# Kernel optimization log

Hardware: AMD Instinct MI355X
Metric: run time of the kernel (lower is better)

Reference implementation:

```python
import jax, jax.numpy as jnp
import numpy as np

V, T_CTX, D, H, L = 32000, 1024, 768, 12, 6
K = D // H  # head_size = 64
EPS = 1e-5


def _ln(x, g, b):
    mu = jnp.mean(x, axis=-1, keepdims=True)
    var = jnp.mean((x - mu) ** 2, axis=-1, keepdims=True)
    return (x - mu) / jnp.sqrt(var + EPS) * g + b


def setup_inputs() -> dict:
    key = jax.random.key(0)
    ks = jax.random.split(key, 24)
    std = 0.02
    B, T = 4, 1024
    inp = {
        "token_ids": jax.random.randint(ks[0], (B, T), 0, V),
        "targets": jax.random.randint(ks[1], (B, T), 0, V),
        "tok_emb": std * jax.random.normal(ks[2], (V, D), jnp.float32),
        "pos_emb": std * jax.random.normal(ks[3], (T_CTX, D), jnp.float32),
        # per-layer stacked params
        "Wq": std * jax.random.normal(ks[4], (L, H, D, K), jnp.float32),
        "Wk": std * jax.random.normal(ks[5], (L, H, D, K), jnp.float32),
        "Wv": std * jax.random.normal(ks[6], (L, H, D, D), jnp.float32),
        "Wproj": std * jax.random.normal(ks[7], (L, H * D, D), jnp.float32),
        "bproj": jnp.zeros((L, D), jnp.float32),
        "ln1_g": jnp.ones((L, D), jnp.float32),
        "ln1_b": jnp.zeros((L, D), jnp.float32),
        "ln2_g": jnp.ones((L, D), jnp.float32),
        "ln2_b": jnp.zeros((L, D), jnp.float32),
        "W1": std * jax.random.normal(ks[8], (L, D, 4 * D), jnp.float32),
        "b1": jnp.zeros((L, 4 * D), jnp.float32),
        "W2": std * jax.random.normal(ks[9], (L, 4 * D, D), jnp.float32),
        "b2": jnp.zeros((L, D), jnp.float32),
        "lnf_g": jnp.ones((D,), jnp.float32),
        "lnf_b": jnp.zeros((D,), jnp.float32),
        "Whead": std * jax.random.normal(ks[10], (D, V), jnp.float32),
        "bhead": jnp.zeros((V,), jnp.float32),
    }
    return inp


def reference(token_ids, targets, tok_emb, pos_emb, Wq, Wk, Wv, Wproj, bproj,
              ln1_g, ln1_b, ln2_g, ln2_b, W1, b1, W2, b2, lnf_g, lnf_b,
              Whead, bhead):
    B, T = token_ids.shape
    x = tok_emb[token_ids] + pos_emb[:T]  # (B,T,D)
    mask = jnp.tril(jnp.ones((T, T), bool))  # causal tril buffer
    scale = 1.0 / np.sqrt(K)
    for l in range(L):
        h = _ln(x, ln1_g[l], ln1_b[l])
        q = jnp.einsum("btd,hdk->bhtk", h, Wq[l])
        k = jnp.einsum("btd,hdk->bhtk", h, Wk[l])
        v = jnp.einsum("btd,hde->bhte", h, Wv[l])  # value proj is D->D per head
        s = jnp.einsum("bhtk,bhsk->bhts", q, k) * scale
        s = jnp.where(mask, s, -jnp.inf)
        a = jax.nn.softmax(s, axis=-1)
        o = jnp.einsum("bhts,bhse->bhte", a, v)  # (B,H,T,D)
        o = o.transpose(0, 2, 1, 3).reshape(B, T, H * D)  # concat heads
        x = x + o @ Wproj[l] + bproj[l]
        h2 = _ln(x, ln2_g[l], ln2_b[l])
        x = x + jax.nn.relu(h2 @ W1[l] + b1[l]) @ W2[l] + b2[l]
    x = _ln(x, lnf_g, lnf_b)
    logits = x @ Whead + bhead  # (B,T,V)
    logp = jax.nn.log_softmax(logits, axis=-1)
    loss = -jnp.take_along_axis(logp, targets[..., None], axis=-1).mean()
    return logits, loss
```

## Files before the change

### kernel.cpp

```cpp
#include <hip/hip_runtime.h>
#include <hip/hip_bf16.h>


#define NBATCH 4
#define TT 1024
#define DD 768
#define NH 12
#define HK 64
#define NL 6
#define NV 32000
#define BT 4096
#define HD 9216
#define FF 3072

using bf16x8 = __attribute__((ext_vector_type(8))) short;
using f32x4  = __attribute__((ext_vector_type(4))) float;

#define GF_OUTBF16 1
#define GF_ACCUM   2
#define GF_BIAS    4
#define GF_RELU    8

__global__ __launch_bounds__(256, 2)
void gemm_kernel(const __hip_bfloat16* __restrict__ A,
                 const __hip_bfloat16* __restrict__ Bt,
                 void* __restrict__ Cv,
                 const float* __restrict__ bias,
                 int Kd, int lda, int ldb, int ldc,
                 int GH,
                 long sA1, long sA2, long sB1, long sB2, long sC1, long sC2,
                 int flags, float scale)
{
    int g  = blockIdx.z;
    int g1 = g / GH, g2 = g % GH;
    const short* Ag = (const short*)A  + g1 * sA1 + g2 * sA2;
    const short* Bg = (const short*)Bt + g1 * sB1 + g2 * sB2;
    long coff = g1 * sC1 + g2 * sC2;
    int n0 = blockIdx.x * 128, m0 = blockIdx.y * 128;

    __shared__ short As[128 * 40];
    __shared__ short Bs[128 * 40];

    int tid  = threadIdx.x;
    int wave = tid >> 6, lane = tid & 63;
    int wm = (wave >> 1) * 64, wn = (wave & 1) * 64;
    int lm = lane & 15, quad = lane >> 4;

    f32x4 acc[4][4];
#pragma unroll
    for (int i = 0; i < 4; i++)
#pragma unroll
        for (int j = 0; j < 4; j++) acc[i][j] = (f32x4){0.f, 0.f, 0.f, 0.f};

    for (int k0 = 0; k0 < Kd; k0 += 32) {
        __syncthreads();
#pragma unroll
        for (int i = 0; i < 2; i++) {
            int c = tid + i * 256;
            int row = c >> 2, kc = (c & 3) << 3;
            *(bf16x8*)(&As[row * 40 + kc]) =
                *(const bf16x8*)(Ag + (long)(m0 + row) * lda + k0 + kc);
            *(bf16x8*)(&Bs[row * 40 + kc]) =
                *(const bf16x8*)(Bg + (long)(n0 + row) * ldb + k0 + kc);
        }
        __syncthreads();

        bf16x8 af[4], bfv[4];
#pragma unroll
        for (int mi = 0; mi < 4; mi++)
            af[mi] = *(const bf16x8*)(&As[(wm + mi * 16 + lm) * 40 + quad * 8]);
#pragma unroll
        for (int ni = 0; ni < 4; ni++)
            bfv[ni] = *(const bf16x8*)(&Bs[(wn + ni * 16 + lm) * 40 + quad * 8]);
#pragma unroll
        for (int mi = 0; mi < 4; mi++)
#pragma unroll
            for (int ni = 0; ni < 4; ni++)
                acc[mi][ni] = __builtin_amdgcn_mfma_f32_16x16x32_bf16(
                    af[mi], bfv[ni], acc[mi][ni], 0, 0, 0);
    }

    bool outbf = flags & GF_OUTBF16;
    bool accum = flags & GF_ACCUM;
    bool hbias = flags & GF_BIAS;
    bool relu  = flags & GF_RELU;
#pragma unroll
    for (int mi = 0; mi < 4; mi++) {
#pragma unroll
        for (int ni = 0; ni < 4; ni++) {
            int colg = n0 + wn + ni * 16 + lm;
            float bv = hbias ? bias[colg] : 0.f;
#pragma unroll
            for (int r = 0; r < 4; r++) {
                int rowg = m0 + wm + mi * 16 + quad * 4 + r;
                float v = acc[mi][ni][r] * scale + bv;
                if (relu) v = fmaxf(v, 0.f);
                long idx = coff + (long)rowg * ldc + colg;
                if (outbf) {
                    ((__hip_bfloat16*)Cv)[idx] = __float2bfloat16(v);
                } else {
                    float* cp = (float*)Cv + idx;
                    *cp = accum ? (*cp + v) : v;
                }
            }
        }
    }
}

__global__ void transpose_kernel(const float* __restrict__ in,
                                 __hip_bfloat16* __restrict__ out,
                                 int R, int C, long inBatch, long outBatch)
{
    __shared__ float tile[32][33];
    long ib = (long)blockIdx.z * inBatch;
    long ob = (long)blockIdx.z * outBatch;
    int c0 = blockIdx.x * 32, r0 = blockIdx.y * 32;
    int tx = threadIdx.x, ty = threadIdx.y;
#pragma unroll
    for (int i = 0; i < 4; i++) {
        int r = r0 + ty + i * 8;
        tile[ty + i * 8][tx] = in[ib + (long)r * C + c0 + tx];
    }
    __syncthreads();
#pragma unroll
    for (int i = 0; i < 4; i++) {
        int c = c0 + ty + i * 8;
        out[ob + (long)c * R + r0 + tx] = __float2bfloat16(tile[tx][ty + i * 8]);
    }
}

__global__ void ln_kernel(const float* __restrict__ x,
                          const float* __restrict__ g,
                          const float* __restrict__ b,
                          __hip_bfloat16* __restrict__ out)
{
    int row = blockIdx.x;
    const float* xp = x + (long)row * DD;
    int tid = threadIdx.x;
    float a0 = xp[tid], a1 = xp[tid + 256], a2 = xp[tid + 512];
    float s = a0 + a1 + a2;
    for (int off = 32; off; off >>= 1) s += __shfl_down(s, off);
    __shared__ float red[4];
    int wave = tid >> 6, lane = tid & 63;
    if (lane == 0) red[wave] = s;
    __syncthreads();
    float mean = (red[0] + red[1] + red[2] + red[3]) * (1.f / DD);
    float d0 = a0 - mean, d1 = a1 - mean, d2 = a2 - mean;
    float vs = d0 * d0 + d1 * d1 + d2 * d2;
    for (int off = 32; off; off >>= 1) vs += __shfl_down(vs, off);
    __syncthreads();
    if (lane == 0) red[wave] = vs;
    __syncthreads();
    float var  = (red[0] + red[1] + red[2] + red[3]) * (1.f / DD);
    float rstd = rsqrtf(var + 1e-5f);
    __hip_bfloat16* op = out + (long)row * DD;
    op[tid]       = __float2bfloat16(d0 * rstd * g[tid]       + b[tid]);
    op[tid + 256] = __float2bfloat16(d1 * rstd * g[tid + 256] + b[tid + 256]);
    op[tid + 512] = __float2bfloat16(d2 * rstd * g[tid + 512] + b[tid + 512]);
}

__global__ void embed_kernel(const int* __restrict__ ids,
                             const float* __restrict__ tok,
                             const float* __restrict__ pos,
                             float* __restrict__ x)
{
    int row = blockIdx.x;
    int t = row & (TT - 1);
    long id = ids[row];
    int tid = threadIdx.x;
    float* xp = x + (long)row * DD;
    const float* tp = tok + id * DD;
    const float* pp = pos + (long)t * DD;
    for (int i = tid; i < DD; i += 256) xp[i] = tp[i] + pp[i];
}

__global__ void causal_softmax_kernel(__hip_bfloat16* __restrict__ S)
{
    long row = blockIdx.x;
    int t = (int)(row & (TT - 1));
    __hip_bfloat16* sp = S + row * TT;
    int tid = threadIdx.x;
    float v[4];
    float mx = -1e30f;
#pragma unroll
    for (int i = 0; i < 4; i++) {
        int c = tid + i * 256;
        float xv = (c <= t) ? __bfloat162float(sp[c]) : -1e30f;
        v[i] = xv;
        mx = fmaxf(mx, xv);
    }
    for (int off = 32; off; off >>= 1) mx = fmaxf(mx, __shfl_down(mx, off));
    __shared__ float red[4];
    int wave = tid >> 6, lane = tid & 63;
    if (lane == 0) red[wave] = mx;
    __syncthreads();
    mx = fmaxf(fmaxf(red[0], red[1]), fmaxf(red[2], red[3]));
    float e[4];
    float sm = 0.f;
#pragma unroll
    for (int i = 0; i < 4; i++) {
        e[i] = (v[i] > -1e29f) ? __expf(v[i] - mx) : 0.f;
        sm += e[i];
    }
    for (int off = 32; off; off >>= 1) sm += __shfl_down(sm, off);
    __syncthreads();
    if (lane == 0) red[wave] = sm;
    __syncthreads();
    sm = red[0] + red[1] + red[2] + red[3];
    float inv = 1.f / sm;
#pragma unroll
    for (int i = 0; i < 4; i++) {
        int c = tid + i * 256;
        sp[c] = __float2bfloat16(e[i] * inv);
    }
}

__global__ void row_loss_kernel(const float* __restrict__ logits,
                                const int* __restrict__ targets,
                                float* __restrict__ rowloss)
{
    int row = blockIdx.x;
    const float* lp = logits + (long)row * NV;
    int tid = threadIdx.x;
    float mx = -1e30f, sm = 0.f;
    for (int i = tid; i < NV; i += 256) {
        float v = lp[i];
        if (v <= mx) sm += __expf(v - mx);
        else { sm = sm * __expf(mx - v) + 1.f; mx = v; }
    }
    for (int off = 32; off; off >>= 1) {
        float mo = __shfl_down(mx, off), so = __shfl_down(sm, off);
        float nm = fmaxf(mx, mo);
        sm = sm * __expf(mx - nm) + so * __expf(mo - nm);
        mx = nm;
    }
    __shared__ float smx[4], ssm[4];
    int wave = tid >> 6, lane = tid & 63;
    if (lane == 0) { smx[wave] = mx; ssm[wave] = sm; }
    __syncthreads();
    if (tid == 0) {
        float M = smx[0], Ssum = ssm[0];
        for (int w = 1; w < 4; w++) {
            float nm = fmaxf(M, smx[w]);
            Ssum = Ssum * __expf(M - nm) + ssm[w] * __expf(smx[w] - nm);
            M = nm;
        }
        float lse = M + logf(Ssum);
        rowloss[row] = lse - lp[targets[row]];
    }
}

__global__ void loss_reduce_kernel(const float* __restrict__ rowloss,
                                   float* __restrict__ out)
{
    int tid = threadIdx.x;
    float s = 0.f;
    for (int i = tid; i < BT; i += 256) s += rowloss[i];
    for (int off = 32; off; off >>= 1) s += __shfl_down(s, off);
    __shared__ float red[4];
    if ((tid & 63) == 0) red[tid >> 6] = s;
    __syncthreads();
    if (tid == 0) out[0] = (red[0] + red[1] + red[2] + red[3]) * (1.f / BT);
}

extern "C" void kernel_launch(void* const* d_in, const int* in_sizes, int n_in,
                              void* d_out, int out_size, void* d_ws, size_t ws_size,
                              hipStream_t stream)
{
    const int*   token_ids = (const int*)  d_in[0];
    const int*   targets   = (const int*)  d_in[1];
    const float* tok_emb   = (const float*)d_in[2];
    const float* pos_emb   = (const float*)d_in[3];
    const float* Wq        = (const float*)d_in[4];
    const float* Wk        = (const float*)d_in[5];
    const float* Wv        = (const float*)d_in[6];
    const float* Wproj     = (const float*)d_in[7];
    const float* bproj     = (const float*)d_in[8];
    const float* ln1_g     = (const float*)d_in[9];
    const float* ln1_b     = (const float*)d_in[10];
    const float* ln2_g     = (const float*)d_in[11];
    const float* ln2_b     = (const float*)d_in[12];
    const float* W1        = (const float*)d_in[13];
    const float* b1        = (const float*)d_in[14];
    const float* W2        = (const float*)d_in[15];
    const float* b2        = (const float*)d_in[16];
    const float* lnf_g     = (const float*)d_in[17];
    const float* lnf_b     = (const float*)d_in[18];
    const float* Whead     = (const float*)d_in[19];
    const float* bhead     = (const float*)d_in[20];

    float* logits   = (float*)d_out;
    float* loss_out = logits + (long)BT * NV;

    char* ws = (char*)d_ws;
    size_t off = 0;
    auto alloc = [&](size_t bytes) {
        size_t p = off;
        off += (bytes + 255) & ~(size_t)255;
        return p;
    };
    float*          x    = (float*)         (ws + alloc((size_t)BT * DD * 4));
    __hip_bfloat16* h    = (__hip_bfloat16*)(ws + alloc((size_t)BT * DD * 2));
    __hip_bfloat16* qb   = (__hip_bfloat16*)(ws + alloc((size_t)BT * DD * 2));
    __hip_bfloat16* kb   = (__hip_bfloat16*)(ws + alloc((size_t)BT * DD * 2));
    __hip_bfloat16* vT   = (__hip_bfloat16*)(ws + alloc((size_t)NBATCH * NH * DD * TT * 2));
    __hip_bfloat16* Sb   = (__hip_bfloat16*)(ws + alloc((size_t)NBATCH * NH * TT * TT * 2));
    __hip_bfloat16* ob   = (__hip_bfloat16*)(ws + alloc((size_t)BT * HD * 2));
    __hip_bfloat16* wT   = (__hip_bfloat16*)(ws + alloc((size_t)NV * DD * 2));
    float*          rowloss = (float*)      (ws + alloc((size_t)BT * 4));

    __hip_bfloat16* mid = Sb;

    __hip_bfloat16* wqT    = wT;
    __hip_bfloat16* wkT    = wqT + (long)DD * DD;
    __hip_bfloat16* wvT    = wkT + (long)DD * DD;
    __hip_bfloat16* wprojT = wvT + (long)NH * DD * DD;
    __hip_bfloat16* w1T    = wprojT + (long)DD * HD;
    __hip_bfloat16* w2T    = w1T + (long)FF * DD;
    __hip_bfloat16* wheadT = wT;

    dim3 tb(32, 8);

    embed_kernel<<<BT, 256, 0, stream>>>(token_ids, tok_emb, pos_emb, x);

    for (int l = 0; l < NL; l++) {
        transpose_kernel<<<dim3(HK / 32, DD / 32, NH), tb, 0, stream>>>(
            Wq + (long)l * NH * DD * HK, wqT, DD, HK, (long)DD * HK, (long)HK * DD);
        transpose_kernel<<<dim3(HK / 32, DD / 32, NH), tb, 0, stream>>>(
            Wk + (long)l * NH * DD * HK, wkT, DD, HK, (long)DD * HK, (long)HK * DD);
        transpose_kernel<<<dim3(DD / 32, DD / 32, NH), tb, 0, stream>>>(
            Wv + (long)l * NH * DD * DD, wvT, DD, DD, (long)DD * DD, (long)DD * DD);
        transpose_kernel<<<dim3(DD / 32, HD / 32, 1), tb, 0, stream>>>(
            Wproj + (long)l * HD * DD, wprojT, HD, DD, 0, 0);
        transpose_kernel<<<dim3(FF / 32, DD / 32, 1), tb, 0, stream>>>(
            W1 + (long)l * DD * FF, w1T, DD, FF, 0, 0);
        transpose_kernel<<<dim3(DD / 32, FF / 32, 1), tb, 0, stream>>>(
            W2 + (long)l * FF * DD, w2T, FF, DD, 0, 0);

        ln_kernel<<<BT, 256, 0, stream>>>(x, ln1_g + l * DD, ln1_b + l * DD, h);

        gemm_kernel<<<dim3(DD / 128, BT / 128, 1), 256, 0, stream>>>(
            h, wqT, qb, nullptr, DD, DD, DD, DD, 1, 0, 0, 0, 0, 0, 0,
            GF_OUTBF16, 1.0f);
        gemm_kernel<<<dim3(DD / 128, BT / 128, 1), 256, 0, stream>>>(
            h, wkT, kb, nullptr, DD, DD, DD, DD, 1, 0, 0, 0, 0, 0, 0,
            GF_OUTBF16, 1.0f);

        gemm_kernel<<<dim3(TT / 128, DD / 128, NBATCH * NH), 256, 0, stream>>>(
            wvT, h, vT, nullptr, DD, DD, DD, TT, NH,
            0, (long)DD * DD,
            (long)TT * DD, 0,
            (long)NH * DD * TT, (long)DD * TT,
            GF_OUTBF16, 1.0f);

        gemm_kernel<<<dim3(TT / 128, TT / 128, NBATCH * NH), 256, 0, stream>>>(
            qb, kb, Sb, nullptr, HK, DD, DD, TT, NH,
            (long)TT * DD, HK,
            (long)TT * DD, HK,
            (long)NH * TT * TT, (long)TT * TT,
            GF_OUTBF16, 0.125f);

        causal_softmax_kernel<<<NBATCH * NH * TT, 256, 0, stream>>>(Sb);

        gemm_kernel<<<dim3(DD / 128, TT / 128, NBATCH * NH), 256, 0, stream>>>(
            Sb, vT, ob, nullptr, TT, TT, TT, HD, NH,
            (long)NH * TT * TT, (long)TT * TT,
            (long)NH * DD * TT, (long)DD * TT,
            (long)TT * HD, DD,
            GF_OUTBF16, 1.0f);

        gemm_kernel<<<dim3(DD / 128, BT / 128, 1), 256, 0, stream>>>(
            ob, wprojT, x, bproj + l * DD, HD, HD, HD, DD, 1,
            0, 0, 0, 0, 0, 0, GF_ACCUM | GF_BIAS, 1.0f);

        ln_kernel<<<BT, 256, 0, stream>>>(x, ln2_g + l * DD, ln2_b + l * DD, h);

        gemm_kernel<<<dim3(FF / 128, BT / 128, 1), 256, 0, stream>>>(
            h, w1T, mid, b1 + (long)l * FF, DD, DD, DD, FF, 1,
            0, 0, 0, 0, 0, 0, GF_OUTBF16 | GF_BIAS | GF_RELU, 1.0f);

        gemm_kernel<<<dim3(DD / 128, BT / 128, 1), 256, 0, stream>>>(
            mid, w2T, x, b2 + l * DD, FF, FF, FF, DD, 1,
            0, 0, 0, 0, 0, 0, GF_ACCUM | GF_BIAS, 1.0f);
    }

    transpose_kernel<<<dim3(NV / 32, DD / 32, 1), tb, 0, stream>>>(
        Whead, wheadT, DD, NV, 0, 0);
    ln_kernel<<<BT, 256, 0, stream>>>(x, lnf_g, lnf_b, h);
    gemm_kernel<<<dim3(NV / 128, BT / 128, 1), 256, 0, stream>>>(
        h, wheadT, logits, bhead, DD, DD, DD, NV, 1,
        0, 0, 0, 0, 0, 0, GF_BIAS, 1.0f);

    row_loss_kernel<<<BT, 256, 0, stream>>>(logits, targets, rowloss);
    loss_reduce_kernel<<<1, 256, 0, stream>>>(rowloss, loss_out);
}
```

Baseline: 6.184 ms.

## Skip masked causal tiles, load tiles via global_load_lds, swizzle head GEMM

```diff
diff --git a/kernel.cpp b/kernel.cpp
--- a/kernel.cpp
+++ b/kernel.cpp
@@ -20,6 +20,9 @@
 #define GF_ACCUM   2
 #define GF_BIAS    4
 #define GF_RELU    8
+#define GF_CAUSAL  16
+#define GF_KTRUNC  32
+#define GF_SWIZZLE 64
 
 __global__ __launch_bounds__(256, 2)
 void gemm_kernel(const __hip_bfloat16* __restrict__ A,
@@ -31,20 +34,37 @@
                  long sA1, long sA2, long sB1, long sB2, long sC1, long sC2,
                  int flags, float scale)
 {
+    int bx = blockIdx.x, by = blockIdx.y;
+    if (flags & GF_SWIZZLE) {
+        int gx = gridDim.x, gy = gridDim.y;
+        int nwg = gx * gy;
+        int id  = by * gx + bx;
+        int q = nwg >> 3, r = nwg & 7;
+        int xcd = id & 7, loc = id >> 3;
+        int sw = (xcd < r) ? xcd * (q + 1) + loc
+                           : r * (q + 1) + (xcd - r) * q + loc;
+        bx = sw % gx;
+        by = sw / gx;
+    }
+    int n0 = bx * 128, m0 = by * 128;
+    if ((flags & GF_CAUSAL) && n0 > m0) return;
+    int Keff = (flags & GF_KTRUNC) ? ((Kd < m0 + 128) ? Kd : m0 + 128) : Kd;
+
     int g  = blockIdx.z;
     int g1 = g / GH, g2 = g % GH;
     const short* Ag = (const short*)A  + g1 * sA1 + g2 * sA2;
     const short* Bg = (const short*)Bt + g1 * sB1 + g2 * sB2;
     long coff = g1 * sC1 + g2 * sC2;
-    int n0 = blockIdx.x * 128, m0 = blockIdx.y * 128;
-
-    __shared__ short As[128 * 40];
-    __shared__ short Bs[128 * 40];
+
+    __shared__ short As[128 * 32];
+    __shared__ short Bs[128 * 32];
 
     int tid  = threadIdx.x;
     int wave = tid >> 6, lane = tid & 63;
     int wm = (wave >> 1) * 64, wn = (wave & 1) * 64;
     int lm = lane & 15, quad = lane >> 4;
+    int srow = lane >> 2;
+    int scol = (lane & 3) << 3;
 
     f32x4 acc[4][4];
 #pragma unroll
@@ -52,26 +72,34 @@
 #pragma unroll
         for (int j = 0; j < 4; j++) acc[i][j] = (f32x4){0.f, 0.f, 0.f, 0.f};
 
-    for (int k0 = 0; k0 < Kd; k0 += 32) {
+    for (int k0 = 0; k0 < Keff; k0 += 32) {
         __syncthreads();
 #pragma unroll
         for (int i = 0; i < 2; i++) {
-            int c = tid + i * 256;
-            int row = c >> 2, kc = (c & 3) << 3;
-            *(bf16x8*)(&As[row * 40 + kc]) =
-                *(const bf16x8*)(Ag + (long)(m0 + row) * lda + k0 + kc);
-            *(bf16x8*)(&Bs[row * 40 + kc]) =
-                *(const bf16x8*)(Bg + (long)(n0 + row) * ldb + k0 + kc);
+            int c   = wave + (i << 2);
+            int row = (c << 4) + srow;
+            __builtin_amdgcn_global_load_lds(
+                (const __attribute__((address_space(1))) void*)
+                    (Ag + (long)(m0 + row) * lda + k0 + scol),
+                (__attribute__((address_space(3))) void*)
+                    (&As[(c << 9) + (lane << 3)]),
+                16, 0, 0);
+            __builtin_amdgcn_global_load_lds(
+                (const __attribute__((address_space(1))) void*)
+                    (Bg + (long)(n0 + row) * ldb + k0 + scol),
+                (__attribute__((address_space(3))) void*)
+                    (&Bs[(c << 9) + (lane << 3)]),
+                16, 0, 0);
         }
         __syncthreads();
 
         bf16x8 af[4], bfv[4];
 #pragma unroll
         for (int mi = 0; mi < 4; mi++)
-            af[mi] = *(const bf16x8*)(&As[(wm + mi * 16 + lm) * 40 + quad * 8]);
+            af[mi] = *(const bf16x8*)(&As[(wm + mi * 16 + lm) * 32 + quad * 8]);
 #pragma unroll
         for (int ni = 0; ni < 4; ni++)
-            bfv[ni] = *(const bf16x8*)(&Bs[(wn + ni * 16 + lm) * 40 + quad * 8]);
+            bfv[ni] = *(const bf16x8*)(&Bs[(wn + ni * 16 + lm) * 32 + quad * 8]);
 #pragma unroll
         for (int mi = 0; mi < 4; mi++)
 #pragma unroll
@@ -98,9 +126,11 @@
                 long idx = coff + (long)rowg * ldc + colg;
                 if (outbf) {
                     ((__hip_bfloat16*)Cv)[idx] = __float2bfloat16(v);
+                } else if (accum) {
+                    float* cp = (float*)Cv + idx;
+                    *cp = *cp + v;
                 } else {
-                    float* cp = (float*)Cv + idx;
-                    *cp = accum ? (*cp + v) : v;
+                    __builtin_nontemporal_store(v, (float*)Cv + idx);
                 }
             }
         }
@@ -178,6 +208,7 @@
 {
     long row = blockIdx.x;
     int t = (int)(row & (TT - 1));
+    int cmax = ((t >> 7) + 1) << 7;
     __hip_bfloat16* sp = S + row * TT;
     int tid = threadIdx.x;
     float v[4];
@@ -185,7 +216,8 @@
 #pragma unroll
     for (int i = 0; i < 4; i++) {
         int c = tid + i * 256;
-        float xv = (c <= t) ? __bfloat162float(sp[c]) : -1e30f;
+        float xv = -1e30f;
+        if (c <= t) xv = __bfloat162float(sp[c]);
         v[i] = xv;
         mx = fmaxf(mx, xv);
     }
@@ -211,7 +243,7 @@
 #pragma unroll
     for (int i = 0; i < 4; i++) {
         int c = tid + i * 256;
-        sp[c] = __float2bfloat16(e[i] * inv);
+        if (c < cmax) sp[c] = __float2bfloat16(e[i] * inv);
     }
 }
 
@@ -358,7 +390,7 @@
             (long)TT * DD, HK,
             (long)TT * DD, HK,
             (long)NH * TT * TT, (long)TT * TT,
-            GF_OUTBF16, 0.125f);
+            GF_OUTBF16 | GF_CAUSAL, 0.125f);
 
         causal_softmax_kernel<<<NBATCH * NH * TT, 256, 0, stream>>>(Sb);
 
@@ -367,7 +399,7 @@
             (long)NH * TT * TT, (long)TT * TT,
             (long)NH * DD * TT, (long)DD * TT,
             (long)TT * HD, DD,
-            GF_OUTBF16, 1.0f);
+            GF_OUTBF16 | GF_KTRUNC, 1.0f);
 
         gemm_kernel<<<dim3(DD / 128, BT / 128, 1), 256, 0, stream>>>(
             ob, wprojT, x, bproj + l * DD, HD, HD, HD, DD, 1,
@@ -389,7 +421,7 @@
     ln_kernel<<<BT, 256, 0, stream>>>(x, lnf_g, lnf_b, h);
     gemm_kernel<<<dim3(NV / 128, BT / 128, 1), 256, 0, stream>>>(
         h, wheadT, logits, bhead, DD, DD, DD, NV, 1,
-        0, 0, 0, 0, 0, 0, GF_BIAS, 1.0f);
+        0, 0, 0, 0, 0, 0, GF_BIAS | GF_SWIZZLE, 1.0f);
 
     row_loss_kernel<<<BT, 256, 0, stream>>>(logits, targets, rowloss);
     loss_reduce_kernel<<<1, 256, 0, stream>>>(rowloss, loss_out);
```

Result: faster. 5.710 ms (-7.7%).
